# Optimization experiments

Hardware: AMD Instinct MI355X
Metric: run time of the kernel (lower is better)

The kernel has to match this reference:

```python
import jax, jax.numpy as jnp
import numpy as np

N_NODES = 100000


def _gcn_aggregate(x, edge_index):
    """Symmetric-normalized GCN aggregation with self-loops (PyG gcn_norm).
    Returns A_hat @ x where A_hat = D^-1/2 (A + I) D^-1/2.
    """
    n = x.shape[0]
    row, col = edge_index[0], edge_index[1]          # messages flow row -> col
    loop = jnp.arange(n, dtype=edge_index.dtype)
    src = jnp.concatenate([row, loop])
    dst = jnp.concatenate([col, loop])
    # degree at target nodes (includes self-loop weight 1)
    deg = jax.ops.segment_sum(jnp.ones(src.shape[0], x.dtype), dst, num_segments=n)
    dinv = jnp.where(deg > 0, jax.lax.rsqrt(deg), 0.0)
    coef = dinv[src] * dinv[dst]                     # [E+N]
    msg = x[src] * coef[:, None]                     # [E+N, F] gather + scale
    return jax.ops.segment_sum(msg, dst, num_segments=n)  # [N, F] scatter-add


def setup_inputs() -> dict:
    key = jax.random.key(0)
    k1, k2, k3, k4 = jax.random.split(key, 4)
    in_size, out_size = 128, 64
    n_edges = 3200000
    x = jax.random.normal(k1, (N_NODES, in_size), dtype=jnp.float32)
    edge_index = jax.random.randint(k2, (2, n_edges), 0, N_NODES, dtype=jnp.int32)
    scale = 1.0 / np.sqrt(in_size)
    W_mu = jax.random.normal(k3, (in_size, out_size), dtype=jnp.float32) * scale
    W_logstd = jax.random.normal(k4, (in_size, out_size), dtype=jnp.float32) * scale
    b_mu = jnp.zeros((out_size,), jnp.float32)
    b_logstd = jnp.zeros((out_size,), jnp.float32)
    return {"x": x, "edge_index": edge_index, "W_mu": W_mu, "b_mu": b_mu,
            "W_logstd": W_logstd, "b_logstd": b_logstd}


def reference(x, edge_index, W_mu, b_mu, W_logstd, b_logstd):
    # Both GCNConv branches share the same normalized aggregation; by linearity
    # (A_hat @ x) @ W == A_hat @ (x @ W), so aggregate once and apply each linear.
    agg = _gcn_aggregate(x, edge_index)              # [N, in_size]
    mu = agg @ W_mu + b_mu                           # [N, out_size]
    logstd = agg @ W_logstd + b_logstd               # [N, out_size]
    return (mu, logstd)
```

## Files before the change

kernel.cpp:

```cpp
#include <hip/hip_runtime.h>

#define F_IN 128
#define F_OUT 64
#define TILE 4096
#define CAP 4608

__device__ inline unsigned short f2bf(float f) {
    unsigned int x = __builtin_bit_cast(unsigned int, f);
    unsigned int r = x + 0x7FFFu + ((x >> 16) & 1u);
    return (unsigned short)(r >> 16);
}

__global__ __launch_bounds__(1024) void repack_dyn(
        const int* __restrict__ row, const int* __restrict__ col,
        int* __restrict__ gcur, int* __restrict__ bpk, int E, int NB) {
    __shared__ __align__(16) int colbuf[TILE];
    __shared__ int cur[1024];
    const int t = threadIdx.x;
    const int tile = blockIdx.x;
    const int base = tile * TILE;
    const int n = min(TILE, E - base);
    const int n4 = n >> 2;
    cur[t] = 0;
    __syncthreads();
    {
        const int4* c4 = (const int4*)(col + base);
        for (int i = t; i < n4; i += 1024) {
            const int4 c = c4[i];
            *(int4*)&colbuf[4 * i] = c;
            atomicAdd(&cur[c.x >> 7], 1);
            atomicAdd(&cur[c.y >> 7], 1);
            atomicAdd(&cur[c.z >> 7], 1);
            atomicAdd(&cur[c.w >> 7], 1);
        }
        for (int i = n4 * 4 + t; i < n; i += 1024) {
            const int c = col[base + i];
            colbuf[i] = c;
            atomicAdd(&cur[c >> 7], 1);
        }
    }
    __syncthreads();
    {
        const int h = cur[t];
        int rb = 0;
        if (t < NB && h > 0) rb = atomicAdd(&gcur[t], h);
        cur[t] = t * CAP + rb;
    }
    __syncthreads();
    {
        const int4* r4 = (const int4*)(row + base);
        for (int i = t; i < n4; i += 1024) {
            const int4 r = r4[i];
            const int cx = colbuf[4 * i + 0];
            const int cy = colbuf[4 * i + 1];
            const int cz = colbuf[4 * i + 2];
            const int cw = colbuf[4 * i + 3];
            const int p0 = atomicAdd(&cur[cx >> 7], 1);
            const int p1 = atomicAdd(&cur[cy >> 7], 1);
            const int p2 = atomicAdd(&cur[cz >> 7], 1);
            const int p3 = atomicAdd(&cur[cw >> 7], 1);
            if (p0 < (cx >> 7) * CAP + CAP) bpk[p0] = r.x | ((cx & 127) << 17);
            if (p1 < (cy >> 7) * CAP + CAP) bpk[p1] = r.y | ((cy & 127) << 17);
            if (p2 < (cz >> 7) * CAP + CAP) bpk[p2] = r.z | ((cz & 127) << 17);
            if (p3 < (cw >> 7) * CAP + CAP) bpk[p3] = r.w | ((cw & 127) << 17);
        }
        for (int i = n4 * 4 + t; i < n; i += 1024) {
            const int c = colbuf[i];
            const int pos = atomicAdd(&cur[c >> 7], 1);
            if (pos < (c >> 7) * CAP + CAP)
                bpk[pos] = row[base + i] | ((c & 127) << 17);
        }
    }
}

__global__ __launch_bounds__(1024) void deg_kernel(
        const int* __restrict__ bpk, const int* __restrict__ totB,
        int* __restrict__ deg, float* __restrict__ dinv, int N) {
    __shared__ int h[128];
    const int b = blockIdx.x;
    const int t = threadIdx.x;
    if (t < 128) h[t] = 0;
    __syncthreads();
    const int tot = min(totB[b], CAP);
    const int4* bp4 = (const int4*)(bpk + b * CAP);
    const int tot4 = tot >> 2;
    for (int i = t; i < tot4; i += 1024) {
        const int4 v = bp4[i];
        atomicAdd(&h[v.x >> 17], 1);
        atomicAdd(&h[v.y >> 17], 1);
        atomicAdd(&h[v.z >> 17], 1);
        atomicAdd(&h[v.w >> 17], 1);
    }
    for (int i = tot4 * 4 + t; i < tot; i += 1024)
        atomicAdd(&h[bpk[b * CAP + i] >> 17], 1);
    __syncthreads();
    const int node = b * 128 + t;
    if (t < 128 && node < N) {
        deg[node] = h[t];
        dinv[node] = rsqrtf((float)h[t] + 1.0f);
    }
}

__global__ __launch_bounds__(256) void gemm_kernel(
        const float* __restrict__ x, const float* __restrict__ Wmu,
        const float* __restrict__ Wls, const float* __restrict__ dinv,
        unsigned int* __restrict__ y, int N) {
    __shared__ __align__(16) float xs[64 * F_IN];
    const int tid = threadIdx.x;
    const int base = blockIdx.x * 64;
    const int nn = min(64, N - base);
    {
        const float4* xg = (const float4*)(x + (size_t)base * F_IN);
        float4* xs4 = (float4*)xs;
        const int cnt = nn * (F_IN / 4);
        for (int i = tid; i < cnt; i += 256) xs4[i] = xg[i];
    }
    __syncthreads();
    const int wv = tid >> 6;
    const int lane = tid & 63;
    const int half = lane >> 5;
    const int lp = lane & 31;
    const int nbase = wv * 16 + half * 8;
    const float* W0 = (lp < 16) ? Wmu : Wls;
    const int coff = (lp < 16) ? (4 * lp) : (4 * (lp - 16));
    float acc[8][4];
#pragma unroll
    for (int n = 0; n < 8; n++)
#pragma unroll
        for (int c = 0; c < 4; c++) acc[n][c] = 0.f;

    for (int k = 0; k < F_IN; k += 4) {
        const float4 w0 = *(const float4*)&W0[(size_t)(k + 0) * F_OUT + coff];
        const float4 w1 = *(const float4*)&W0[(size_t)(k + 1) * F_OUT + coff];
        const float4 w2 = *(const float4*)&W0[(size_t)(k + 2) * F_OUT + coff];
        const float4 w3 = *(const float4*)&W0[(size_t)(k + 3) * F_OUT + coff];
#pragma unroll
        for (int n = 0; n < 8; n++) {
            const float4 xv = *(const float4*)&xs[(nbase + n) * F_IN + k];
            acc[n][0] = fmaf(xv.x, w0.x, acc[n][0]);
            acc[n][1] = fmaf(xv.x, w0.y, acc[n][1]);
            acc[n][2] = fmaf(xv.x, w0.z, acc[n][2]);
            acc[n][3] = fmaf(xv.x, w0.w, acc[n][3]);
            acc[n][0] = fmaf(xv.y, w1.x, acc[n][0]);
            acc[n][1] = fmaf(xv.y, w1.y, acc[n][1]);
            acc[n][2] = fmaf(xv.y, w1.z, acc[n][2]);
            acc[n][3] = fmaf(xv.y, w1.w, acc[n][3]);
            acc[n][0] = fmaf(xv.z, w2.x, acc[n][0]);
            acc[n][1] = fmaf(xv.z, w2.y, acc[n][1]);
            acc[n][2] = fmaf(xv.z, w2.z, acc[n][2]);
            acc[n][3] = fmaf(xv.z, w2.w, acc[n][3]);
            acc[n][0] = fmaf(xv.w, w3.x, acc[n][0]);
            acc[n][1] = fmaf(xv.w, w3.y, acc[n][1]);
            acc[n][2] = fmaf(xv.w, w3.z, acc[n][2]);
            acc[n][3] = fmaf(xv.w, w3.w, acc[n][3]);
        }
    }
    const int ci = (lp < 16) ? (2 * lp) : (32 + 2 * (lp - 16));
#pragma unroll
    for (int n = 0; n < 8; n++) {
        const int node = base + nbase + n;
        if (node < N) {
            const float dv = dinv[node];
            const unsigned u0 = (unsigned)f2bf(acc[n][0] * dv) |
                                ((unsigned)f2bf(acc[n][1] * dv) << 16);
            const unsigned u1 = (unsigned)f2bf(acc[n][2] * dv) |
                                ((unsigned)f2bf(acc[n][3] * dv) << 16);
            *(uint2*)&y[(size_t)node * 64 + ci] = make_uint2(u0, u1);
        }
    }
}

__global__ __launch_bounds__(1024) void bucket_gather(
        const int* __restrict__ bpk, const int* __restrict__ deg,
        const uint4* __restrict__ Y4,
        const float* __restrict__ bmu, const float* __restrict__ bls,
        float* __restrict__ out, int N) {
    __shared__ int elist[CAP];
    __shared__ int hN[128];
    __shared__ int nodebase[128];
    __shared__ int cursor[128];
    __shared__ float dinv_s[128];
    __shared__ int w0sum;
    const int b = blockIdx.x;
    const int t = threadIdx.x;
    const int lane = t & 63;

    int hv = 0;
    if (t < 128) {
        const int node = b * 128 + t;
        hv = (node < N) ? deg[node] : 0;
        dinv_s[t] = rsqrtf((float)hv + 1.0f);
        hN[t] = hv;
    }
    int x = hv;
#pragma unroll
    for (int off = 1; off < 64; off <<= 1) {
        const int y = __shfl_up(x, off, 64);
        if (lane >= off) x += y;
    }
    if (t == 63) w0sum = x;
    __syncthreads();
    if (t >= 64 && t < 128) x += w0sum;
    if (t < 128) { nodebase[t] = x - hv; cursor[t] = x - hv; }
    __syncthreads();
    const int tot = min(nodebase[127] + hN[127], CAP);

    const int4* bp4 = (const int4*)(bpk + b * CAP);
    const int tot4 = tot >> 2;
    for (int i = t; i < tot4; i += 1024) {
        const int4 v = bp4[i];
        int p0 = atomicAdd(&cursor[v.x >> 17], 1);
        int p1 = atomicAdd(&cursor[v.y >> 17], 1);
        int p2 = atomicAdd(&cursor[v.z >> 17], 1);
        int p3 = atomicAdd(&cursor[v.w >> 17], 1);
        if (p0 < CAP) elist[p0] = v.x & 0x1FFFF;
        if (p1 < CAP) elist[p1] = v.y & 0x1FFFF;
        if (p2 < CAP) elist[p2] = v.z & 0x1FFFF;
        if (p3 < CAP) elist[p3] = v.w & 0x1FFFF;
    }
    for (int i = tot4 * 4 + t; i < tot; i += 1024) {
        const int p = bpk[b * CAP + i];
        const int pos = atomicAdd(&cursor[p >> 17], 1);
        if (pos < CAP) elist[pos] = p & 0x1FFFF;
    }
    __syncthreads();

    const int w = t >> 6;
    const int eg = lane >> 4;
    const int q = lane & 15;

#define ACC(u)                                                        \
    do {                                                              \
        A.x += __builtin_bit_cast(float, (u).x << 16);                \
        A.y += __builtin_bit_cast(float, (u).x & 0xFFFF0000u);        \
        A.z += __builtin_bit_cast(float, (u).y << 16);                \
        A.w += __builtin_bit_cast(float, (u).y & 0xFFFF0000u);        \
        B.x += __builtin_bit_cast(float, (u).z << 16);                \
        B.y += __builtin_bit_cast(float, (u).z & 0xFFFF0000u);        \
        B.z += __builtin_bit_cast(float, (u).w << 16);                \
        B.w += __builtin_bit_cast(float, (u).w & 0xFFFF0000u);        \
    } while (0)

    for (int nid = w * 8; nid < w * 8 + 8; nid++) {
        const int node = b * 128 + nid;
        if (node >= N) continue;
        const int cnt = hN[nid];
        const int nb_ = nodebase[nid];
        float4 A = make_float4(0.f, 0.f, 0.f, 0.f);
        float4 B = make_float4(0.f, 0.f, 0.f, 0.f);
        int e = 0;
        for (; e + 16 <= cnt; e += 16) {
            const int s0 = elist[nb_ + e + 0 + eg];
            const int s1 = elist[nb_ + e + 4 + eg];
            const int s2 = elist[nb_ + e + 8 + eg];
            const int s3 = elist[nb_ + e + 12 + eg];
            const uint4 u0 = Y4[(size_t)s0 * 16 + q];
            const uint4 u1 = Y4[(size_t)s1 * 16 + q];
            const uint4 u2 = Y4[(size_t)s2 * 16 + q];
            const uint4 u3 = Y4[(size_t)s3 * 16 + q];
            ACC(u0); ACC(u1); ACC(u2); ACC(u3);
        }
        for (; e < cnt; e += 4) {
            if (e + eg < cnt) {
                const int s0 = elist[nb_ + e + eg];
                const uint4 u0 = Y4[(size_t)s0 * 16 + q];
                ACC(u0);
            }
        }
        A.x += __shfl_xor(A.x, 16); A.y += __shfl_xor(A.y, 16);
        A.z += __shfl_xor(A.z, 16); A.w += __shfl_xor(A.w, 16);
        B.x += __shfl_xor(B.x, 16); B.y += __shfl_xor(B.y, 16);
        B.z += __shfl_xor(B.z, 16); B.w += __shfl_xor(B.w, 16);
        A.x += __shfl_xor(A.x, 32); A.y += __shfl_xor(A.y, 32);
        A.z += __shfl_xor(A.z, 32); A.w += __shfl_xor(A.w, 32);
        B.x += __shfl_xor(B.x, 32); B.y += __shfl_xor(B.y, 32);
        B.z += __shfl_xor(B.z, 32); B.w += __shfl_xor(B.w, 32);
        {
            const uint4 u = Y4[(size_t)node * 16 + q];
            ACC(u);
        }
        const float dv = dinv_s[nid];
        if (lane < 16) {
            if (q < 8) {
                const float4 b0 = ((const float4*)bmu)[2 * q];
                const float4 b1 = ((const float4*)bmu)[2 * q + 1];
                float* o = out + (size_t)node * F_OUT + q * 8;
                *(float4*)o = make_float4(b0.x + A.x * dv, b0.y + A.y * dv,
                                          b0.z + A.z * dv, b0.w + A.w * dv);
                *(float4*)(o + 4) = make_float4(b1.x + B.x * dv, b1.y + B.y * dv,
                                                b1.z + B.z * dv, b1.w + B.w * dv);
            } else {
                const float4 b0 = ((const float4*)bls)[2 * (q - 8)];
                const float4 b1 = ((const float4*)bls)[2 * (q - 8) + 1];
                float* o = out + ((size_t)N + node) * F_OUT + (q - 8) * 8;
                *(float4*)o = make_float4(b0.x + A.x * dv, b0.y + A.y * dv,
                                          b0.z + A.z * dv, b0.w + A.w * dv);
                *(float4*)(o + 4) = make_float4(b1.x + B.x * dv, b1.y + B.y * dv,
                                                b1.z + B.z * dv, b1.w + B.w * dv);
            }
        }
    }
#undef ACC
}

extern "C" void kernel_launch(void* const* d_in, const int* in_sizes, int n_in,
                              void* d_out, int out_size, void* d_ws, size_t ws_size,
                              hipStream_t stream) {
    const float* x   = (const float*)d_in[0];
    const int*   ei  = (const int*)d_in[1];
    const float* Wmu = (const float*)d_in[2];
    const float* bmu = (const float*)d_in[3];
    const float* Wls = (const float*)d_in[4];
    const float* bls = (const float*)d_in[5];
    float* out = (float*)d_out;

    const int N = in_sizes[0] / F_IN;
    const int E = in_sizes[1] / 2;
    const int* row = ei;
    const int* col = ei + E;
    const int NB = (N + 127) >> 7;
    const int NT = (E + TILE - 1) / TILE;
    const int CAPTOT = NB * CAP;

    char* p = (char*)d_ws;
    auto alloc = [&](size_t bytes) {
        char* r = p;
        p += (bytes + 511) & ~(size_t)511;
        return r;
    };
    int*   gcur  = (int*)  alloc((size_t)NB * 4);
    int*   bpk   = (int*)  alloc((size_t)CAPTOT * 4 + 4096);
    int*   deg   = (int*)  alloc((size_t)N * 4);
    float* dinv  = (float*)alloc((size_t)N * 4);
    unsigned int* y = (unsigned int*)alloc((size_t)N * F_IN * 2);

    hipMemsetAsync(gcur, 0, (size_t)NB * 4, stream);
    repack_dyn<<<NT, 1024, 0, stream>>>(row, col, gcur, bpk, E, NB);
    deg_kernel<<<NB, 1024, 0, stream>>>(bpk, gcur, deg, dinv, N);
    gemm_kernel<<<(N + 63) / 64, 256, 0, stream>>>(x, Wmu, Wls, dinv, y, N);
    bucket_gather<<<NB, 1024, 0, stream>>>(bpk, deg, (const uint4*)y,
                                           bmu, bls, out, N);
}
```

Measured before the change: 319.3 us.

## Fuse degree histogram into GEMM kernel and pad bucket counters

```diff
diff --git a/kernel.cpp b/kernel.cpp
--- a/kernel.cpp
+++ b/kernel.cpp
@@ -43,7 +43,7 @@
     {
         const int h = cur[t];
         int rb = 0;
-        if (t < NB && h > 0) rb = atomicAdd(&gcur[t], h);
+        if (t < NB && h > 0) rb = atomicAdd(&gcur[t * 16], h);
         cur[t] = t * CAP + rb;
     }
     __syncthreads();
@@ -73,51 +73,52 @@
     }
 }
 
-__global__ __launch_bounds__(1024) void deg_kernel(
-        const int* __restrict__ bpk, const int* __restrict__ totB,
-        int* __restrict__ deg, float* __restrict__ dinv, int N) {
+__global__ __launch_bounds__(512) void deg_gemm_kernel(
+        const int* __restrict__ bpk, const int* __restrict__ gcur,
+        const float* __restrict__ x, const float* __restrict__ Wmu,
+        const float* __restrict__ Wls,
+        int* __restrict__ deg, unsigned int* __restrict__ y, int N) {
+    __shared__ __align__(16) float xs[128 * F_IN];
     __shared__ int h[128];
+    __shared__ float dinv_s[128];
     const int b = blockIdx.x;
     const int t = threadIdx.x;
+    const int base = b * 128;
+    const int nn = min(128, N - base);
+
     if (t < 128) h[t] = 0;
     __syncthreads();
-    const int tot = min(totB[b], CAP);
-    const int4* bp4 = (const int4*)(bpk + b * CAP);
-    const int tot4 = tot >> 2;
-    for (int i = t; i < tot4; i += 1024) {
-        const int4 v = bp4[i];
-        atomicAdd(&h[v.x >> 17], 1);
-        atomicAdd(&h[v.y >> 17], 1);
-        atomicAdd(&h[v.z >> 17], 1);
-        atomicAdd(&h[v.w >> 17], 1);
-    }
-    for (int i = tot4 * 4 + t; i < tot; i += 1024)
-        atomicAdd(&h[bpk[b * CAP + i] >> 17], 1);
-    __syncthreads();
-    const int node = b * 128 + t;
-    if (t < 128 && node < N) {
-        deg[node] = h[t];
-        dinv[node] = rsqrtf((float)h[t] + 1.0f);
-    }
-}
-
-__global__ __launch_bounds__(256) void gemm_kernel(
-        const float* __restrict__ x, const float* __restrict__ Wmu,
-        const float* __restrict__ Wls, const float* __restrict__ dinv,
-        unsigned int* __restrict__ y, int N) {
-    __shared__ __align__(16) float xs[64 * F_IN];
-    const int tid = threadIdx.x;
-    const int base = blockIdx.x * 64;
-    const int nn = min(64, N - base);
+    {
+        const int tot = min(gcur[b * 16], CAP);
+        const int4* bp4 = (const int4*)(bpk + b * CAP);
+        const int tot4 = tot >> 2;
+        for (int i = t; i < tot4; i += 512) {
+            const int4 v = bp4[i];
+            atomicAdd(&h[v.x >> 17], 1);
+            atomicAdd(&h[v.y >> 17], 1);
+            atomicAdd(&h[v.z >> 17], 1);
+            atomicAdd(&h[v.w >> 17], 1);
+        }
+        for (int i = tot4 * 4 + t; i < tot; i += 512)
+            atomicAdd(&h[bpk[b * CAP + i] >> 17], 1);
+    }
     {
         const float4* xg = (const float4*)(x + (size_t)base * F_IN);
         float4* xs4 = (float4*)xs;
         const int cnt = nn * (F_IN / 4);
-        for (int i = tid; i < cnt; i += 256) xs4[i] = xg[i];
-    }
-    __syncthreads();
-    const int wv = tid >> 6;
-    const int lane = tid & 63;
+        for (int i = t; i < cnt; i += 512) xs4[i] = xg[i];
+    }
+    __syncthreads();
+    if (t < 128) {
+        const int node = base + t;
+        const float dv = rsqrtf((float)h[t] + 1.0f);
+        dinv_s[t] = dv;
+        if (node < N) deg[node] = h[t];
+    }
+    __syncthreads();
+
+    const int wv = t >> 6;
+    const int lane = t & 63;
     const int half = lane >> 5;
     const int lp = lane & 31;
     const int nbase = wv * 16 + half * 8;
@@ -160,7 +161,7 @@
     for (int n = 0; n < 8; n++) {
         const int node = base + nbase + n;
         if (node < N) {
-            const float dv = dinv[node];
+            const float dv = dinv_s[nbase + n];
             const unsigned u0 = (unsigned)f2bf(acc[n][0] * dv) |
                                 ((unsigned)f2bf(acc[n][1] * dv) << 16);
             const unsigned u1 = (unsigned)f2bf(acc[n][2] * dv) |
@@ -328,16 +329,14 @@
         p += (bytes + 511) & ~(size_t)511;
         return r;
     };
-    int*   gcur  = (int*)  alloc((size_t)NB * 4);
+    int*   gcur  = (int*)  alloc((size_t)NB * 16 * 4);
     int*   bpk   = (int*)  alloc((size_t)CAPTOT * 4 + 4096);
     int*   deg   = (int*)  alloc((size_t)N * 4);
-    float* dinv  = (float*)alloc((size_t)N * 4);
     unsigned int* y = (unsigned int*)alloc((size_t)N * F_IN * 2);
 
-    hipMemsetAsync(gcur, 0, (size_t)NB * 4, stream);
+    hipMemsetAsync(gcur, 0, (size_t)NB * 16 * 4, stream);
     repack_dyn<<<NT, 1024, 0, stream>>>(row, col, gcur, bpk, E, NB);
-    deg_kernel<<<NB, 1024, 0, stream>>>(bpk, gcur, deg, dinv, N);
-    gemm_kernel<<<(N + 63) / 64, 256, 0, stream>>>(x, Wmu, Wls, dinv, y, N);
+    deg_gemm_kernel<<<NB, 512, 0, stream>>>(bpk, gcur, x, Wmu, Wls, deg, y, N);
     bucket_gather<<<NB, 1024, 0, stream>>>(bpk, deg, (const uint4*)y,
                                            bmu, bls, out, N);
 }
```

New measurement: 336.9 us. 1.05x slower.
